# Kernel tuning notes

Measured on AMD Instinct MI355X. Metric: run time of the kernel, lower is better.

## Reference

```python
import jax, jax.numpy as jnp
import numpy as np

LEAK = 0.2  # tf.nn.leaky_relu default alpha

def leaky(x):
    return jnp.where(x >= 0, x, LEAK * x)

def dense(x, W, b):
    return leaky(x @ W + b)

def lstm_seq(x, Wk, Wr, b):
    # Keras LSTM, gate order [i, f, c, o]; recurrent_activation=sigmoid,
    # activation=leaky_relu (applied to candidate and to c for h).
    B, T, _ = x.shape
    H = Wr.shape[0]
    zx = jnp.einsum('btd,dh->bth', x, Wk) + b  # precompute input projections
    def step(carry, z_t):
        h, c = carry
        z = z_t + h @ Wr
        i, f, g, o = jnp.split(z, 4, axis=-1)
        c = jax.nn.sigmoid(f) * c + jax.nn.sigmoid(i) * leaky(g)
        h = jax.nn.sigmoid(o) * leaky(c)
        return (h, c), h
    init = (jnp.zeros((B, H), x.dtype), jnp.zeros((B, H), x.dtype))
    _, hs = jax.lax.scan(step, init, jnp.swapaxes(zx, 0, 1))  # [T,B,H]
    return jnp.swapaxes(hs, 0, 1)  # [B,T,H]

def setup_inputs() -> dict:
    key = jax.random.key(0)
    ks = iter(jax.random.split(key, 32))
    B, T, F, H = 32, 4096, 11, 128
    data = jax.random.uniform(next(ks), (B, T, F), dtype=jnp.float32)
    def p(i, o):
        W = jax.random.normal(next(ks), (i, o), jnp.float32) * (1.0 / np.sqrt(i))
        return W, jnp.zeros((o,), jnp.float32)
    W_M1, b_M1 = p(6, 8);   W_M2, b_M2 = p(8, 16)
    W_T1, b_T1 = p(11, 8);  W_T2, b_T2 = p(8, 16)
    W_S1, b_S1 = p(58, 32); W_S2, b_S2 = p(32, 64)
    Wk, _ = p(124, 4 * H); Wr, _ = p(H, 4 * H)
    b_l = jnp.zeros((4 * H,), jnp.float32)
    W_P1, b_P1 = p(H, 64); W_P2, b_P2 = p(64, 32)
    W_P3, b_P3 = p(32, 16); W_P4, b_P4 = p(16, 8); W_P5, b_P5 = p(8, 3)
    return dict(data=data, W_M1=W_M1, b_M1=b_M1, W_M2=W_M2, b_M2=b_M2,
                W_T1=W_T1, b_T1=b_T1, W_T2=W_T2, b_T2=b_T2,
                W_S1=W_S1, b_S1=b_S1, W_S2=W_S2, b_S2=b_S2,
                Wk=Wk, Wr=Wr, b_l=b_l,
                W_P1=W_P1, b_P1=b_P1, W_P2=W_P2, b_P2=b_P2,
                W_P3=W_P3, b_P3=b_P3, W_P4=W_P4, b_P4=b_P4,
                W_P5=W_P5, b_P5=b_P5)

def reference(data, W_M1, b_M1, W_M2, b_M2, W_T1, b_T1, W_T2, b_T2,
              W_S1, b_S1, W_S2, b_S2, Wk, Wr, b_l,
              W_P1, b_P1, W_P2, b_P2, W_P3, b_P3, W_P4, b_P4, W_P5, b_P5):
    body = data[:, :, 4:10]
    env = data[:, :, 1:4]
    Ta = data[:, :, 1:2]
    Pa = jnp.log1p(Ta)
    # M tower (dropout is identity at inference)
    M = dense(dense(body, W_M1, b_M1), W_M2, b_M2)
    # Tsk tower with abs
    Tsk = jnp.abs(dense(data, W_T1, b_T1))
    Tsk = jnp.abs(dense(Tsk, W_T2, b_T2))
    Psk = jnp.log1p(Tsk)
    # per-sample concat loops == batched concat on last axis
    s_in = jnp.concatenate([M, Tsk, Psk, Pa, env, body], axis=-1)  # [B,T,58]
    S = dense(dense(s_in, W_S1, b_S1), W_S2, b_S2)  # [B,T,64]
    lstm_in = jnp.concatenate([M, Tsk, Psk, Pa, S, data], axis=-1)  # [B,T,124]
    h = lstm_seq(lstm_in, Wk, Wr, b_l)  # [B,T,128]
    d = dense(h, W_P1, b_P1)
    d = dense(d, W_P2, b_P2)
    d = dense(d, W_P3, b_P3)
    d = dense(d, W_P4, b_P4)
    d = dense(d, W_P5, b_P5)
    out = jax.nn.softmax(d, axis=-1)
    output = out[:, 2:3, :]  # [B,1,3]
    x = jnp.concatenate([data[:, 2:3, 1:], output], axis=-1).reshape(32, 1, 13)
    return (output, x)
```

## Files before the change

kernel.cpp:

```cpp
#include <hip/hip_runtime.h>
#include <math.h>

#define LEAK 0.2f

__device__ __forceinline__ float leaky_f(float x) { return x >= 0.0f ? x : LEAK * x; }
__device__ __forceinline__ float sigmoid_f(float x) { return 1.0f / (1.0f + expf(-x)); }

__global__ __launch_bounds__(512)
void lstm_cls_kernel(const float* __restrict__ data,
                     const float* __restrict__ W_M1, const float* __restrict__ b_M1,
                     const float* __restrict__ W_M2, const float* __restrict__ b_M2,
                     const float* __restrict__ W_T1, const float* __restrict__ b_T1,
                     const float* __restrict__ W_T2, const float* __restrict__ b_T2,
                     const float* __restrict__ W_S1, const float* __restrict__ b_S1,
                     const float* __restrict__ W_S2, const float* __restrict__ b_S2,
                     const float* __restrict__ Wk,   const float* __restrict__ b_l,
                     const float* __restrict__ Wr,
                     const float* __restrict__ W_P1, const float* __restrict__ b_P1,
                     const float* __restrict__ W_P2, const float* __restrict__ b_P2,
                     const float* __restrict__ W_P3, const float* __restrict__ b_P3,
                     const float* __restrict__ W_P4, const float* __restrict__ b_P4,
                     const float* __restrict__ W_P5, const float* __restrict__ b_P5,
                     float* __restrict__ out)
{
    __shared__ float sdata[3][11];
    __shared__ float feat[3][124];
    __shared__ float m1s[3][8];
    __shared__ float t1s[3][8];
    __shared__ float s1s[3][32];
    __shared__ float zx[3][512];
    __shared__ float zs[4][128];
    __shared__ float h[128];
    __shared__ float pp[8][64];
    __shared__ float d1[64], d2[32], d3[16], d4[8];
    __shared__ float sm[3];

    const int b   = blockIdx.x;
    const int tid = threadIdx.x;
    const float* db = data + (size_t)b * 4096 * 11;

    if (tid < 33) {
        int t = tid / 11, k = tid % 11;
        float v = db[t * 11 + k];
        sdata[t][k] = v;
        feat[t][113 + k] = v;
    }

    float pf = 0.0f;
    #pragma unroll 16
    for (int i = 0; i < 128; ++i) pf += Wr[i * 512 + tid];
    #pragma unroll
    for (int i = 0; i < 16; ++i)  pf += W_P1[i * 512 + tid];
    #pragma unroll
    for (int i = 0; i < 4; ++i)   pf += W_P2[i * 512 + tid];

    __syncthreads();

    if (tid < 24) {
        int t = tid / 8, j = tid % 8;
        float acc = b_M1[j];
        for (int k = 0; k < 6; ++k) acc += sdata[t][4 + k] * W_M1[k * 8 + j];
        m1s[t][j] = leaky_f(acc);
    } else if (tid < 48) {
        int u = tid - 24, t = u / 8, j = u % 8;
        float acc = b_T1[j];
        for (int k = 0; k < 11; ++k) acc += sdata[t][k] * W_T1[k * 8 + j];
        t1s[t][j] = fabsf(leaky_f(acc));
    } else if (tid < 51) {
        int t = tid - 48;
        feat[t][48] = log1pf(sdata[t][1]);
    }
    __syncthreads();

    if (tid < 48) {
        int t = tid / 16, j = tid % 16;
        float acc = b_M2[j];
        for (int k = 0; k < 8; ++k) acc += m1s[t][k] * W_M2[k * 16 + j];
        feat[t][j] = leaky_f(acc);
    } else if (tid < 96) {
        int u = tid - 48, t = u / 16, j = u % 16;
        float acc = b_T2[j];
        for (int k = 0; k < 8; ++k) acc += t1s[t][k] * W_T2[k * 16 + j];
        float v = fabsf(leaky_f(acc));
        feat[t][16 + j] = v;
        feat[t][32 + j] = log1pf(v);
    }
    __syncthreads();

    if (tid < 96) {
        int t = tid / 32, j = tid % 32;
        float acc = b_S1[j];
        for (int k = 0; k < 49; ++k) acc += feat[t][k] * W_S1[k * 32 + j];
        for (int k = 0; k < 3;  ++k) acc += sdata[t][1 + k] * W_S1[(49 + k) * 32 + j];
        for (int k = 0; k < 6;  ++k) acc += sdata[t][4 + k] * W_S1[(52 + k) * 32 + j];
        s1s[t][j] = leaky_f(acc);
    }
    __syncthreads();

    if (tid < 192) {
        int t = tid / 64, j = tid % 64;
        float acc = b_S2[j];
        for (int k = 0; k < 32; ++k) acc += s1s[t][k] * W_S2[k * 64 + j];
        feat[t][49 + j] = leaky_f(acc);
    }
    __syncthreads();

    {
        const int col = tid;
        float a0 = b_l[col], a1 = a0, a2 = a0;
        #pragma unroll 4
        for (int k = 0; k < 124; ++k) {
            float w = Wk[k * 512 + col];
            a0 += feat[0][k] * w;
            a1 += feat[1][k] * w;
            a2 += feat[2][k] * w;
        }
        zx[0][col] = a0; zx[1][col] = a1; zx[2][col] = a2;
    }
    if (tid < 128) h[tid] = 0.0f;
    float c = 0.0f;
    const int g = tid >> 7, j = tid & 127;
    __syncthreads();

    for (int t = 0; t < 3; ++t) {
        float z = zx[t][(g << 7) + j];
        if (t > 0) {
            #pragma unroll 8
            for (int k = 0; k < 128; ++k)
                z += h[k] * Wr[k * 512 + (g << 7) + j];
        }
        zs[g][j] = z;
        __syncthreads();
        if (g == 0) {
            float zi = zs[0][j], zf = zs[1][j], zg = zs[2][j], zo = zs[3][j];
            c = sigmoid_f(zf) * c + sigmoid_f(zi) * leaky_f(zg);
            h[j] = sigmoid_f(zo) * leaky_f(c);
        }
        __syncthreads();
    }

    {
        int part = tid >> 6, jj = tid & 63;
        float acc = 0.0f;
        for (int k = part * 16; k < part * 16 + 16; ++k)
            acc += h[k] * W_P1[k * 64 + jj];
        pp[part][jj] = acc;
    }
    __syncthreads();
    if (tid < 64) {
        float acc = b_P1[tid];
        for (int p = 0; p < 8; ++p) acc += pp[p][tid];
        d1[tid] = leaky_f(acc);
    }
    __syncthreads();

    if (tid < 256) {
        int part = tid >> 5, jj = tid & 31;
        float acc = 0.0f;
        for (int k = part * 8; k < part * 8 + 8; ++k)
            acc += d1[k] * W_P2[k * 32 + jj];
        pp[part][jj] = acc;
    }
    __syncthreads();
    if (tid < 32) {
        float acc = b_P2[tid];
        for (int p = 0; p < 8; ++p) acc += pp[p][tid];
        d2[tid] = leaky_f(acc);
    }
    __syncthreads();

    if (tid < 128) {
        int part = tid >> 4, jj = tid & 15;
        float acc = 0.0f;
        for (int k = part * 4; k < part * 4 + 4; ++k)
            acc += d2[k] * W_P3[k * 16 + jj];
        pp[part][jj] = acc;
    }
    __syncthreads();
    if (tid < 16) {
        float acc = b_P3[tid];
        for (int p = 0; p < 8; ++p) acc += pp[p][tid];
        d3[tid] = leaky_f(acc);
    }
    __syncthreads();

    if (tid < 8) {
        float acc = b_P4[tid];
        for (int k = 0; k < 16; ++k) acc += d3[k] * W_P4[k * 8 + tid];
        d4[tid] = leaky_f(acc);
    }
    __syncthreads();

    if (tid == 0) {
        float l[3], mx = -1e30f;
        for (int r = 0; r < 3; ++r) {
            float acc = b_P5[r];
            for (int k = 0; k < 8; ++k) acc += d4[k] * W_P5[k * 3 + r];
            l[r] = leaky_f(acc);
            mx = fmaxf(mx, l[r]);
        }
        float s = 0.0f;
        for (int r = 0; r < 3; ++r) { l[r] = expf(l[r] - mx); s += l[r]; }
        float inv = 1.0f / s;
        for (int r = 0; r < 3; ++r) sm[r] = l[r] * inv;
    }
    __syncthreads();

    if (tid < 3)  out[b * 3 + tid] = sm[tid];
    if (tid < 13) {
        float v = (tid < 10) ? sdata[2][1 + tid] : sm[tid - 10];
        out[96 + b * 13 + tid] = v;
    }

    if (pf == -1234.5678f && sdata[2][0] == -99999.0f) out[0] = pf;
}

extern "C" void kernel_launch(void* const* d_in, const int* in_sizes, int n_in,
                              void* d_out, int out_size, void* d_ws, size_t ws_size,
                              hipStream_t stream) {
    const float* data = (const float*)d_in[0];
    const float* W_M1 = (const float*)d_in[1];
    const float* b_M1 = (const float*)d_in[2];
    const float* W_M2 = (const float*)d_in[3];
    const float* b_M2 = (const float*)d_in[4];
    const float* W_T1 = (const float*)d_in[5];
    const float* b_T1 = (const float*)d_in[6];
    const float* W_T2 = (const float*)d_in[7];
    const float* b_T2 = (const float*)d_in[8];
    const float* W_S1 = (const float*)d_in[9];
    const float* b_S1 = (const float*)d_in[10];
    const float* W_S2 = (const float*)d_in[11];
    const float* b_S2 = (const float*)d_in[12];
    const float* Wk   = (const float*)d_in[13];
    const float* Wr   = (const float*)d_in[14];
    const float* b_l  = (const float*)d_in[15];
    const float* W_P1 = (const float*)d_in[16];
    const float* b_P1 = (const float*)d_in[17];
    const float* W_P2 = (const float*)d_in[18];
    const float* b_P2 = (const float*)d_in[19];
    const float* W_P3 = (const float*)d_in[20];
    const float* b_P3 = (const float*)d_in[21];
    const float* W_P4 = (const float*)d_in[22];
    const float* b_P4 = (const float*)d_in[23];
    const float* W_P5 = (const float*)d_in[24];
    const float* b_P5 = (const float*)d_in[25];
    float* out = (float*)d_out;

    lstm_cls_kernel<<<dim3(32), dim3(512), 0, stream>>>(
        data, W_M1, b_M1, W_M2, b_M2, W_T1, b_T1, W_T2, b_T2,
        W_S1, b_S1, W_S2, b_S2, Wk, b_l, Wr,
        W_P1, b_P1, W_P2, b_P2, W_P3, b_P3, W_P4, b_P4, W_P5, b_P5,
        out);
}
```

Measured before the change: 129.6 us.

## Run feature towers on one wave while other waves prefetch all weights

```diff
diff --git a/kernel.cpp b/kernel.cpp
--- a/kernel.cpp
+++ b/kernel.cpp
@@ -5,6 +5,12 @@
 
 __device__ __forceinline__ float leaky_f(float x) { return x >= 0.0f ? x : LEAK * x; }
 __device__ __forceinline__ float sigmoid_f(float x) { return 1.0f / (1.0f + expf(-x)); }
+
+__device__ __forceinline__ void wave_lds_fence() {
+    __builtin_amdgcn_wave_barrier();
+    __threadfence_block();
+    __builtin_amdgcn_wave_barrier();
+}
 
 __global__ __launch_bounds__(512)
 void lstm_cls_kernel(const float* __restrict__ data,
@@ -39,76 +45,103 @@
     const int tid = threadIdx.x;
     const float* db = data + (size_t)b * 4096 * 11;
 
-    if (tid < 33) {
-        int t = tid / 11, k = tid % 11;
-        float v = db[t * 11 + k];
-        sdata[t][k] = v;
-        feat[t][113 + k] = v;
-    }
-
     float pf = 0.0f;
-    #pragma unroll 16
-    for (int i = 0; i < 128; ++i) pf += Wr[i * 512 + tid];
-    #pragma unroll
-    for (int i = 0; i < 16; ++i)  pf += W_P1[i * 512 + tid];
-    #pragma unroll
-    for (int i = 0; i < 4; ++i)   pf += W_P2[i * 512 + tid];
-
-    __syncthreads();
-
-    if (tid < 24) {
-        int t = tid / 8, j = tid % 8;
-        float acc = b_M1[j];
-        for (int k = 0; k < 6; ++k) acc += sdata[t][4 + k] * W_M1[k * 8 + j];
-        m1s[t][j] = leaky_f(acc);
-    } else if (tid < 48) {
-        int u = tid - 24, t = u / 8, j = u % 8;
-        float acc = b_T1[j];
-        for (int k = 0; k < 11; ++k) acc += sdata[t][k] * W_T1[k * 8 + j];
-        t1s[t][j] = fabsf(leaky_f(acc));
-    } else if (tid < 51) {
-        int t = tid - 48;
-        feat[t][48] = log1pf(sdata[t][1]);
-    }
-    __syncthreads();
-
-    if (tid < 48) {
-        int t = tid / 16, j = tid % 16;
-        float acc = b_M2[j];
-        for (int k = 0; k < 8; ++k) acc += m1s[t][k] * W_M2[k * 16 + j];
-        feat[t][j] = leaky_f(acc);
-    } else if (tid < 96) {
-        int u = tid - 48, t = u / 16, j = u % 16;
-        float acc = b_T2[j];
-        for (int k = 0; k < 8; ++k) acc += t1s[t][k] * W_T2[k * 16 + j];
-        float v = fabsf(leaky_f(acc));
-        feat[t][16 + j] = v;
-        feat[t][32 + j] = log1pf(v);
-    }
-    __syncthreads();
-
-    if (tid < 96) {
-        int t = tid / 32, j = tid % 32;
-        float acc = b_S1[j];
-        for (int k = 0; k < 49; ++k) acc += feat[t][k] * W_S1[k * 32 + j];
-        for (int k = 0; k < 3;  ++k) acc += sdata[t][1 + k] * W_S1[(49 + k) * 32 + j];
-        for (int k = 0; k < 6;  ++k) acc += sdata[t][4 + k] * W_S1[(52 + k) * 32 + j];
-        s1s[t][j] = leaky_f(acc);
-    }
-    __syncthreads();
-
-    if (tid < 192) {
-        int t = tid / 64, j = tid % 64;
-        float acc = b_S2[j];
-        for (int k = 0; k < 32; ++k) acc += s1s[t][k] * W_S2[k * 64 + j];
-        feat[t][49 + j] = leaky_f(acc);
-    }
+
+    if (tid < 64) {
+        if (tid < 33) {
+            int t = tid / 11, k = tid % 11;
+            float v = db[t * 11 + k];
+            sdata[t][k] = v;
+            feat[t][113 + k] = v;
+        }
+        wave_lds_fence();
+
+        if (tid < 24) {
+            int t = tid / 8, j = tid % 8;
+            float acc = b_M1[j];
+            for (int k = 0; k < 6; ++k) acc += sdata[t][4 + k] * W_M1[k * 8 + j];
+            m1s[t][j] = leaky_f(acc);
+        } else if (tid < 48) {
+            int u = tid - 24, t = u / 8, j = u % 8;
+            float acc = b_T1[j];
+            for (int k = 0; k < 11; ++k) acc += sdata[t][k] * W_T1[k * 8 + j];
+            t1s[t][j] = fabsf(leaky_f(acc));
+        } else if (tid < 51) {
+            int t = tid - 48;
+            feat[t][48] = log1pf(sdata[t][1]);
+        }
+        wave_lds_fence();
+
+        for (int idx = tid; idx < 96; idx += 64) {
+            int t, j;
+            if (idx < 48) {
+                t = idx / 16; j = idx % 16;
+                float acc = b_M2[j];
+                for (int k = 0; k < 8; ++k) acc += m1s[t][k] * W_M2[k * 16 + j];
+                feat[t][j] = leaky_f(acc);
+            } else {
+                int u = idx - 48; t = u / 16; j = u % 16;
+                float acc = b_T2[j];
+                for (int k = 0; k < 8; ++k) acc += t1s[t][k] * W_T2[k * 16 + j];
+                float v = fabsf(leaky_f(acc));
+                feat[t][16 + j] = v;
+                feat[t][32 + j] = log1pf(v);
+            }
+        }
+        wave_lds_fence();
+
+        for (int idx = tid; idx < 96; idx += 64) {
+            int t = idx / 32, j = idx % 32;
+            float acc = b_S1[j];
+            for (int k = 0; k < 49; ++k) acc += feat[t][k] * W_S1[k * 32 + j];
+            for (int k = 0; k < 3;  ++k) acc += sdata[t][1 + k] * W_S1[(49 + k) * 32 + j];
+            for (int k = 0; k < 6;  ++k) acc += sdata[t][4 + k] * W_S1[(52 + k) * 32 + j];
+            s1s[t][j] = leaky_f(acc);
+        }
+        wave_lds_fence();
+
+        for (int idx = tid; idx < 192; idx += 64) {
+            int t = idx / 64, j = idx % 64;
+            float acc = b_S2[j];
+            for (int k = 0; k < 32; ++k) acc += s1s[t][k] * W_S2[k * 64 + j];
+            feat[t][49 + j] = leaky_f(acc);
+        }
+    } else {
+        const int widx = tid - 64;
+        float4 a = make_float4(0.f, 0.f, 0.f, 0.f);
+        const float4* p;
+        p = (const float4*)b_l;
+        for (int i = widx; i < 128;   i += 448) { float4 v = p[i]; a.x+=v.x; a.y+=v.y; a.z+=v.z; a.w+=v.w; }
+        p = (const float4*)W_S1;
+        for (int i = widx; i < 464;   i += 448) { float4 v = p[i]; a.x+=v.x; a.y+=v.y; a.z+=v.z; a.w+=v.w; }
+        p = (const float4*)W_S2;
+        for (int i = widx; i < 512;   i += 448) { float4 v = p[i]; a.x+=v.x; a.y+=v.y; a.z+=v.z; a.w+=v.w; }
+        p = (const float4*)Wk;
+        for (int i = widx; i < 15872; i += 448) { float4 v = p[i]; a.x+=v.x; a.y+=v.y; a.z+=v.z; a.w+=v.w; }
+        p = (const float4*)Wr;
+        for (int i = widx; i < 16384; i += 448) { float4 v = p[i]; a.x+=v.x; a.y+=v.y; a.z+=v.z; a.w+=v.w; }
+        p = (const float4*)W_P1;
+        for (int i = widx; i < 2048;  i += 448) { float4 v = p[i]; a.x+=v.x; a.y+=v.y; a.z+=v.z; a.w+=v.w; }
+        p = (const float4*)W_P2;
+        for (int i = widx; i < 512;   i += 448) { float4 v = p[i]; a.x+=v.x; a.y+=v.y; a.z+=v.z; a.w+=v.w; }
+        p = (const float4*)W_P3;
+        for (int i = widx; i < 128;   i += 448) { float4 v = p[i]; a.x+=v.x; a.y+=v.y; a.z+=v.z; a.w+=v.w; }
+        p = (const float4*)W_P4;
+        for (int i = widx; i < 32;    i += 448) { float4 v = p[i]; a.x+=v.x; a.y+=v.y; a.z+=v.z; a.w+=v.w; }
+        p = (const float4*)W_P5;
+        for (int i = widx; i < 6;     i += 448) { float4 v = p[i]; a.x+=v.x; a.y+=v.y; a.z+=v.z; a.w+=v.w; }
+        pf = a.x + a.y + a.z + a.w;
+    }
+
+    if (tid < 128) h[tid] = 0.0f;
+    float c = 0.0f;
+    const int g = tid >> 7, j = tid & 127;
     __syncthreads();
 
     {
         const int col = tid;
         float a0 = b_l[col], a1 = a0, a2 = a0;
-        #pragma unroll 4
+        #pragma unroll 8
         for (int k = 0; k < 124; ++k) {
             float w = Wk[k * 512 + col];
             a0 += feat[0][k] * w;
@@ -117,9 +150,6 @@
         }
         zx[0][col] = a0; zx[1][col] = a1; zx[2][col] = a2;
     }
-    if (tid < 128) h[tid] = 0.0f;
-    float c = 0.0f;
-    const int g = tid >> 7, j = tid & 127;
     __syncthreads();
 
     for (int t = 0; t < 3; ++t) {
```

Result: slower. 137.7 us (+6.3%).

## Preload recurrent weights into registers and head weights into LDS, vectorize projections

Applied to the files above, without the earlier changes.

```diff
diff --git a/kernel.cpp b/kernel.cpp
--- a/kernel.cpp
+++ b/kernel.cpp
@@ -5,6 +5,19 @@
 
 __device__ __forceinline__ float leaky_f(float x) { return x >= 0.0f ? x : LEAK * x; }
 __device__ __forceinline__ float sigmoid_f(float x) { return 1.0f / (1.0f + expf(-x)); }
+
+#define OP1 0
+#define OP2 8192
+#define OP3 10240
+#define OP4 10752
+#define OP5 10880
+#define OB1 10904
+#define OB2 10968
+#define OB3 11000
+#define OB4 11016
+#define OBL 11024
+#define OB5 11536
+#define WLS_N 11540
 
 __global__ __launch_bounds__(512)
 void lstm_cls_kernel(const float* __restrict__ data,
@@ -28,15 +41,19 @@
     __shared__ float m1s[3][8];
     __shared__ float t1s[3][8];
     __shared__ float s1s[3][32];
+    __shared__ float dpart[8][3][32];
+    __shared__ float epart[4][3][64];
+    __shared__ float zpart[4][3][512];
     __shared__ float zx[3][512];
-    __shared__ float zs[4][128];
     __shared__ float h[128];
     __shared__ float pp[8][64];
-    __shared__ float d1[64], d2[32], d3[16], d4[8];
-    __shared__ float sm[3];
+    __shared__ float d1[64], d2[32], d3[16], d4[8], smx[3];
+    __shared__ float wls[WLS_N];
 
     const int b   = blockIdx.x;
     const int tid = threadIdx.x;
+    const int q   = tid >> 7;
+    const int c4  = tid & 127;
     const float* db = data + (size_t)b * 4096 * 11;
 
     if (tid < 33) {
@@ -46,25 +63,64 @@
         feat[t][113 + k] = v;
     }
 
-    float pf = 0.0f;
-    #pragma unroll 16
-    for (int i = 0; i < 128; ++i) pf += Wr[i * 512 + tid];
+    const float4* Wr4 = (const float4*)Wr;
+    float4 rw[32];
     #pragma unroll
-    for (int i = 0; i < 16; ++i)  pf += W_P1[i * 512 + tid];
-    #pragma unroll
-    for (int i = 0; i < 4; ++i)   pf += W_P2[i * 512 + tid];
-
-    __syncthreads();
-
+    for (int kk = 0; kk < 32; ++kk)
+        rw[kk] = Wr4[(32 * q + kk) * 128 + c4];
+
+    float wB[11]; float bBv = 0.0f;
+    float wC[8];  float bCv = 0.0f;
+    float bs1v = 0.0f, bs2v = 0.0f;
     if (tid < 24) {
-        int t = tid / 8, j = tid % 8;
-        float acc = b_M1[j];
-        for (int k = 0; k < 6; ++k) acc += sdata[t][4 + k] * W_M1[k * 8 + j];
+        int j = tid & 7; bBv = b_M1[j];
+        #pragma unroll
+        for (int k = 0; k < 6; ++k) wB[k] = W_M1[k * 8 + j];
+    } else if (tid < 48) {
+        int j = (tid - 24) & 7; bBv = b_T1[j];
+        #pragma unroll
+        for (int k = 0; k < 11; ++k) wB[k] = W_T1[k * 8 + j];
+    }
+    if (tid < 48) {
+        int j = tid & 15; bCv = b_M2[j];
+        #pragma unroll
+        for (int k = 0; k < 8; ++k) wC[k] = W_M2[k * 16 + j];
+    } else if (tid < 96) {
+        int j = (tid - 48) & 15; bCv = b_T2[j];
+        #pragma unroll
+        for (int k = 0; k < 8; ++k) wC[k] = W_T2[k * 16 + j];
+    }
+    if (tid < 96)  bs1v = b_S1[tid & 31];
+    if (tid < 192) bs2v = b_S2[tid & 63];
+
+    if (tid >= 192) {
+        int wi = tid - 192;
+        float4* wls4 = (float4*)wls;
+        for (int i = wi; i < 2048; i += 320) wls4[OP1/4 + i] = ((const float4*)W_P1)[i];
+        for (int i = wi; i < 512;  i += 320) wls4[OP2/4 + i] = ((const float4*)W_P2)[i];
+        for (int i = wi; i < 128;  i += 320) wls4[OP3/4 + i] = ((const float4*)W_P3)[i];
+        for (int i = wi; i < 32;   i += 320) wls4[OP4/4 + i] = ((const float4*)W_P4)[i];
+        for (int i = wi; i < 6;    i += 320) wls4[OP5/4 + i] = ((const float4*)W_P5)[i];
+        for (int i = wi; i < 16;   i += 320) wls4[OB1/4 + i] = ((const float4*)b_P1)[i];
+        for (int i = wi; i < 8;    i += 320) wls4[OB2/4 + i] = ((const float4*)b_P2)[i];
+        for (int i = wi; i < 4;    i += 320) wls4[OB3/4 + i] = ((const float4*)b_P3)[i];
+        for (int i = wi; i < 2;    i += 320) wls4[OB4/4 + i] = ((const float4*)b_P4)[i];
+        for (int i = wi; i < 128;  i += 320) wls4[OBL/4 + i] = ((const float4*)b_l)[i];
+        if (wi < 3) wls[OB5 + wi] = b_P5[wi];
+    }
+    __syncthreads();
+
+    if (tid < 24) {
+        int t = tid / 8, j = tid & 7;
+        float acc = bBv;
+        #pragma unroll
+        for (int k = 0; k < 6; ++k) acc += sdata[t][4 + k] * wB[k];
         m1s[t][j] = leaky_f(acc);
     } else if (tid < 48) {
-        int u = tid - 24, t = u / 8, j = u % 8;
-        float acc = b_T1[j];
-        for (int k = 0; k < 11; ++k) acc += sdata[t][k] * W_T1[k * 8 + j];
+        int u = tid - 24, t = u / 8, j = u & 7;
+        float acc = bBv;
+        #pragma unroll
+        for (int k = 0; k < 11; ++k) acc += sdata[t][k] * wB[k];
         t1s[t][j] = fabsf(leaky_f(acc));
     } else if (tid < 51) {
         int t = tid - 48;
@@ -73,66 +129,124 @@
     __syncthreads();
 
     if (tid < 48) {
-        int t = tid / 16, j = tid % 16;
-        float acc = b_M2[j];
-        for (int k = 0; k < 8; ++k) acc += m1s[t][k] * W_M2[k * 16 + j];
+        int t = tid / 16, j = tid & 15;
+        float acc = bCv;
+        #pragma unroll
+        for (int k = 0; k < 8; ++k) acc += m1s[t][k] * wC[k];
         feat[t][j] = leaky_f(acc);
     } else if (tid < 96) {
-        int u = tid - 48, t = u / 16, j = u % 16;
-        float acc = b_T2[j];
-        for (int k = 0; k < 8; ++k) acc += t1s[t][k] * W_T2[k * 16 + j];
+        int u = tid - 48, t = u / 16, j = u & 15;
+        float acc = bCv;
+        #pragma unroll
+        for (int k = 0; k < 8; ++k) acc += t1s[t][k] * wC[k];
         float v = fabsf(leaky_f(acc));
         feat[t][16 + j] = v;
         feat[t][32 + j] = log1pf(v);
     }
     __syncthreads();
 
+    if (tid < 192) {
+        int kk = tid & 7, j4 = (tid >> 3) & 7, t = tid >> 6;
+        int k0 = kk * 8, k1 = k0 + 8; if (k1 > 58) k1 = 58;
+        const float4* WS1_4 = (const float4*)W_S1;
+        float4 a = make_float4(0.f, 0.f, 0.f, 0.f);
+        for (int k = k0; k < k1; ++k) {
+            float4 w = WS1_4[k * 8 + j4];
+            float sv = (k < 49) ? feat[t][k] : sdata[t][k - 48];
+            a.x = fmaf(sv, w.x, a.x); a.y = fmaf(sv, w.y, a.y);
+            a.z = fmaf(sv, w.z, a.z); a.w = fmaf(sv, w.w, a.w);
+        }
+        ((float4*)&dpart[kk][t][0])[j4] = a;
+    }
+    __syncthreads();
     if (tid < 96) {
-        int t = tid / 32, j = tid % 32;
-        float acc = b_S1[j];
-        for (int k = 0; k < 49; ++k) acc += feat[t][k] * W_S1[k * 32 + j];
-        for (int k = 0; k < 3;  ++k) acc += sdata[t][1 + k] * W_S1[(49 + k) * 32 + j];
-        for (int k = 0; k < 6;  ++k) acc += sdata[t][4 + k] * W_S1[(52 + k) * 32 + j];
+        int t = tid >> 5, j = tid & 31;
+        float acc = bs1v;
+        #pragma unroll
+        for (int kk = 0; kk < 8; ++kk) acc += dpart[kk][t][j];
         s1s[t][j] = leaky_f(acc);
     }
     __syncthreads();
 
     if (tid < 192) {
-        int t = tid / 64, j = tid % 64;
-        float acc = b_S2[j];
-        for (int k = 0; k < 32; ++k) acc += s1s[t][k] * W_S2[k * 64 + j];
+        int kk = tid & 3, j4 = (tid >> 2) & 15, t = tid >> 6;
+        const float4* WS2_4 = (const float4*)W_S2;
+        float4 a = make_float4(0.f, 0.f, 0.f, 0.f);
+        #pragma unroll
+        for (int i = 0; i < 8; ++i) {
+            int k = 8 * kk + i;
+            float4 w = WS2_4[k * 16 + j4];
+            float sv = s1s[t][k];
+            a.x = fmaf(sv, w.x, a.x); a.y = fmaf(sv, w.y, a.y);
+            a.z = fmaf(sv, w.z, a.z); a.w = fmaf(sv, w.w, a.w);
+        }
+        ((float4*)&epart[kk][t][0])[j4] = a;
+    }
+    __syncthreads();
+    if (tid < 192) {
+        int t = tid >> 6, j = tid & 63;
+        float acc = bs2v;
+        #pragma unroll
+        for (int kk = 0; kk < 4; ++kk) acc += epart[kk][t][j];
         feat[t][49 + j] = leaky_f(acc);
     }
     __syncthreads();
 
     {
-        const int col = tid;
-        float a0 = b_l[col], a1 = a0, a2 = a0;
-        #pragma unroll 4
-        for (int k = 0; k < 124; ++k) {
-            float w = Wk[k * 512 + col];
-            a0 += feat[0][k] * w;
-            a1 += feat[1][k] * w;
-            a2 += feat[2][k] * w;
-        }
-        zx[0][col] = a0; zx[1][col] = a1; zx[2][col] = a2;
-    }
-    if (tid < 128) h[tid] = 0.0f;
+        const float4* Wk4 = (const float4*)Wk;
+        float4 f0 = make_float4(0.f,0.f,0.f,0.f), f1 = f0, f2 = f0;
+        #pragma unroll
+        for (int i = 0; i < 31; ++i) {
+            int k = 31 * q + i;
+            float4 w = Wk4[k * 128 + c4];
+            float a = feat[0][k], bb = feat[1][k], cc = feat[2][k];
+            f0.x = fmaf(a,  w.x, f0.x); f0.y = fmaf(a,  w.y, f0.y);
+            f0.z = fmaf(a,  w.z, f0.z); f0.w = fmaf(a,  w.w, f0.w);
+            f1.x = fmaf(bb, w.x, f1.x); f1.y = fmaf(bb, w.y, f1.y);
+            f1.z = fmaf(bb, w.z, f1.z); f1.w = fmaf(bb, w.w, f1.w);
+            f2.x = fmaf(cc, w.x, f2.x); f2.y = fmaf(cc, w.y, f2.y);
+            f2.z = fmaf(cc, w.z, f2.z); f2.w = fmaf(cc, w.w, f2.w);
+        }
+        ((float4*)&zpart[q][0][0])[c4] = f0;
+        ((float4*)&zpart[q][1][0])[c4] = f1;
+        ((float4*)&zpart[q][2][0])[c4] = f2;
+    }
+    __syncthreads();
+    #pragma unroll
+    for (int t = 0; t < 3; ++t) {
+        int col = tid;
+        zx[t][col] = wls[OBL + col] + zpart[0][t][col] + zpart[1][t][col]
+                   + zpart[2][t][col] + zpart[3][t][col];
+    }
+    __syncthreads();
+
     float c = 0.0f;
-    const int g = tid >> 7, j = tid & 127;
-    __syncthreads();
-
-    for (int t = 0; t < 3; ++t) {
-        float z = zx[t][(g << 7) + j];
-        if (t > 0) {
-            #pragma unroll 8
-            for (int k = 0; k < 128; ++k)
-                z += h[k] * Wr[k * 512 + (g << 7) + j];
-        }
-        zs[g][j] = z;
+    if (tid < 128) {
+        float zi = zx[0][tid], zf = zx[0][128 + tid];
+        float zg = zx[0][256 + tid], zo = zx[0][384 + tid];
+        (void)zf;
+        c = sigmoid_f(zi) * leaky_f(zg);
+        h[tid] = sigmoid_f(zo) * leaky_f(c);
+    }
+    __syncthreads();
+    for (int t = 1; t < 3; ++t) {
+        float4 acc = make_float4(0.f, 0.f, 0.f, 0.f);
+        #pragma unroll
+        for (int kk = 0; kk < 32; ++kk) {
+            float hk = h[32 * q + kk];
+            acc.x = fmaf(hk, rw[kk].x, acc.x);
+            acc.y = fmaf(hk, rw[kk].y, acc.y);
+            acc.z = fmaf(hk, rw[kk].z, acc.z);
+            acc.w = fmaf(hk, rw[kk].w, acc.w);
+        }
+        ((float4*)&zpart[q][0][0])[c4] = acc;
         __syncthreads();
-        if (g == 0) {
-            float zi = zs[0][j], zf = zs[1][j], zg = zs[2][j], zo = zs[3][j];
+        if (tid < 128) {
+            int j = tid;
+            float zi = zx[t][j]       + zpart[0][0][j]       + zpart[1][0][j]       + zpart[2][0][j]       + zpart[3][0][j];
+            float zf = zx[t][128 + j] + zpart[0][0][128 + j] + zpart[1][0][128 + j] + zpart[2][0][128 + j] + zpart[3][0][128 + j];
+            float zg = zx[t][256 + j] + zpart[0][0][256 + j] + zpart[1][0][256 + j] + zpart[2][0][256 + j] + zpart[3][0][256 + j];
+            float zo = zx[t][384 + j] + zpart[0][0][384 + j] + zpart[1][0][384 + j] + zpart[2][0][384 + j] + zpart[3][0][384 + j];
             c = sigmoid_f(zf) * c + sigmoid_f(zi) * leaky_f(zg);
             h[j] = sigmoid_f(zo) * leaky_f(c);
         }
@@ -142,77 +256,88 @@
     {
         int part = tid >> 6, jj = tid & 63;
         float acc = 0.0f;
-        for (int k = part * 16; k < part * 16 + 16; ++k)
-            acc += h[k] * W_P1[k * 64 + jj];
+        #pragma unroll
+        for (int i = 0; i < 16; ++i) {
+            int k = part * 16 + i;
+            acc = fmaf(h[k], wls[OP1 + k * 64 + jj], acc);
+        }
         pp[part][jj] = acc;
     }
     __syncthreads();
     if (tid < 64) {
-        float acc = b_P1[tid];
+        float acc = wls[OB1 + tid];
+        #pragma unroll
         for (int p = 0; p < 8; ++p) acc += pp[p][tid];
         d1[tid] = leaky_f(acc);
     }
     __syncthreads();
-
     if (tid < 256) {
         int part = tid >> 5, jj = tid & 31;
         float acc = 0.0f;
-        for (int k = part * 8; k < part * 8 + 8; ++k)
-            acc += d1[k] * W_P2[k * 32 + jj];
+        #pragma unroll
+        for (int i = 0; i < 8; ++i) {
+            int k = part * 8 + i;
+            acc = fmaf(d1[k], wls[OP2 + k * 32 + jj], acc);
+        }
         pp[part][jj] = acc;
     }
     __syncthreads();
     if (tid < 32) {
-        float acc = b_P2[tid];
+        float acc = wls[OB2 + tid];
+        #pragma unroll
         for (int p = 0; p < 8; ++p) acc += pp[p][tid];
         d2[tid] = leaky_f(acc);
     }
     __syncthreads();
-
     if (tid < 128) {
         int part = tid >> 4, jj = tid & 15;
         float acc = 0.0f;
-        for (int k = part * 4; k < part * 4 + 4; ++k)
-            acc += d2[k] * W_P3[k * 16 + jj];
+        #pragma unroll
+        for (int i = 0; i < 4; ++i) {
+            int k = part * 4 + i;
+            acc = fmaf(d2[k], wls[OP3 + k * 16 + jj], acc);
+        }
         pp[part][jj] = acc;
     }
     __syncthreads();
     if (tid < 16) {
-        float acc = b_P3[tid];
+        float acc = wls[OB3 + tid];
+        #pragma unroll
         for (int p = 0; p < 8; ++p) acc += pp[p][tid];
         d3[tid] = leaky_f(acc);
     }
     __syncthreads();
-
     if (tid < 8) {
-        float acc = b_P4[tid];
-        for (int k = 0; k < 16; ++k) acc += d3[k] * W_P4[k * 8 + tid];
+        float acc = wls[OB4 + tid];
+        #pragma unroll
+        for (int k = 0; k < 16; ++k) acc = fmaf(d3[k], wls[OP4 + k * 8 + tid], acc);
         d4[tid] = leaky_f(acc);
     }
     __syncthreads();
-
     if (tid == 0) {
         float l[3], mx = -1e30f;
+        #pragma unroll
         for (int r = 0; r < 3; ++r) {
-            float acc = b_P5[r];
-            for (int k = 0; k < 8; ++k) acc += d4[k] * W_P5[k * 3 + r];
+            float acc = wls[OB5 + r];
+            #pragma unroll
+            for (int k = 0; k < 8; ++k) acc = fmaf(d4[k], wls[OP5 + k * 3 + r], acc);
             l[r] = leaky_f(acc);
             mx = fmaxf(mx, l[r]);
         }
         float s = 0.0f;
+        #pragma unroll
         for (int r = 0; r < 3; ++r) { l[r] = expf(l[r] - mx); s += l[r]; }
         float inv = 1.0f / s;
-        for (int r = 0; r < 3; ++r) sm[r] = l[r] * inv;
-    }
-    __syncthreads();
-
-    if (tid < 3)  out[b * 3 + tid] = sm[tid];
+        #pragma unroll
+        for (int r = 0; r < 3; ++r) smx[r] = l[r] * inv;
+    }
+    __syncthreads();
+
+    if (tid < 3)  out[b * 3 + tid] = smx[tid];
     if (tid < 13) {
-        float v = (tid < 10) ? sdata[2][1 + tid] : sm[tid - 10];
+        float v = (tid < 10) ? sdata[2][1 + tid] : smx[tid - 10];
         out[96 + b * 13 + tid] = v;
     }
-
-    if (pf == -1234.5678f && sdata[2][0] == -99999.0f) out[0] = pf;
 }
 
 extern "C" void kernel_launch(void* const* d_in, const int* in_sizes, int n_in,
```

Result: faster. 123.9 us (-4.3%).
